# Kernel optimization log

Hardware: AMD Instinct MI355X
Metric: run time of the kernel (lower is better)

## Reference

```python
import jax, jax.numpy as jnp
import numpy as np

BATCH = 8192
GROUPS = 512
ARITY = 3
OUT_DIM = 8
ACT_FACTOR = 1.0


def setup_inputs() -> dict:
    key = jax.random.key(0)
    k1, k2 = jax.random.split(key)
    X = jax.random.normal(k1, (BATCH, GROUPS * ARITY), dtype=jnp.float32)
    params = jax.random.normal(k2, (GROUPS, 3 ** ARITY, OUT_DIM), dtype=jnp.float32)
    return {"X": X, "params": params}


def _high_order_act_b(A, params):
    # A: [B, G, r], params: [G, 3**r, D]
    r = A.shape[2]
    ref_ind = (3 ** r - 1) // 2  # sum_{i<r} 3**i
    A_abs = jnp.abs(A)
    A_ind = jnp.argsort(A_abs, axis=2)                      # [B,G,r] int
    A_sort = jnp.take_along_axis(A_abs, A_ind, axis=2)      # sorted |A|
    sgn = jnp.where(A >= 0, 1, -1).astype(jnp.int32)
    A_sgn = jnp.take_along_axis(sgn, A_ind, axis=2)         # signs in sorted order
    # simplex interpolation coefficients: smallest |A| then successive diffs
    coef = jnp.concatenate(
        [A_sort[:, :, :1], A_sort[:, :, 1:] - A_sort[:, :, :-1]], axis=2
    )  # [B,G,r]
    # base-3 index: suffix cumsum of sign * 3**orig_index, offset to center
    terms = A_sgn * (3 ** A_ind.astype(jnp.int32))
    params_A_ind = jnp.flip(jnp.cumsum(jnp.flip(terms, axis=2), axis=2), axis=2) + ref_ind  # [B,G,r]
    idx = jnp.transpose(params_A_ind, (1, 0, 2))            # [G,B,r]
    # gather params[g, idx[g,b,k], :] -> [G,B,r,D]
    gathered = jnp.take_along_axis(params[:, None, :, :], idx[..., None], axis=2)
    # einsum 'jikl,ijk->ijl' (torch) == 'gbrd,bgr->bgd'
    return jnp.einsum('gbrd,bgr->bgd', gathered, coef)


def reference(X, params):
    B = X.shape[0]
    A = X.reshape(B, GROUPS, ARITY)
    out1 = _high_order_act_b(A, params)                     # [B,G,D]
    return out1.reshape(B, GROUPS * OUT_DIM) * ACT_FACTOR
```

## Files before the change

### kernel.cpp

```cpp
#include <hip/hip_runtime.h>

typedef float vf4 __attribute__((ext_vector_type(4)));

#define BATCH  8192
#define GROUPS 512
#define OUT_D  8
#define GCH    32
#define NCH    (GROUPS / GCH)
#define RT     64
#define PQ     54
#define LQ     55

__global__ __launch_bounds__(256) void hoact_kernel(
    const float* __restrict__ X,
    const float* __restrict__ P,
    float* __restrict__ out)
{
    __shared__ vf4 lp[GCH * LQ];

    const int chunk = blockIdx.x % NCH;
    const int rt    = blockIdx.x / NCH;

    const int tid  = threadIdx.x;
    const int lane = tid & 63;
    const int w    = tid >> 6;
    const int gsub = lane >> 1;
    const int h    = lane & 1;

    const vf4* P4 = (const vf4*)P + (size_t)chunk * (GCH * PQ);
    #pragma unroll
    for (int k = 0; k < 7; ++k) {
        int m = tid + 256 * k;
        if (m < GCH * PQ) {
            int gq = m / PQ;
            int iq = m - gq * PQ;
            lp[gq * LQ + iq] = P4[m];
        }
    }
    __syncthreads();

    const int g = chunk * GCH + gsub;
    const float* xcol = X + (size_t)g * 3;
    vf4* outb = (vf4*)out + (size_t)chunk * (GCH * OUT_D / 4) + lane;
    const size_t row_u = GROUPS * OUT_D / 4;
    const int base = gsub * LQ + h;

    #pragma unroll
    for (int it = 0; it < RT / 4; ++it) {
        const int row = rt * RT + w * (RT / 4) + it;

        const float* xp = xcol + (size_t)row * (GROUPS * 3);
        float x0 = xp[0], x1 = xp[1], x2 = xp[2];

        float b0 = fabsf(x0), b1 = fabsf(x1), b2 = fabsf(x2);
        int t0 = (x0 >= 0.f) ? 1 : -1;
        int t1 = (x1 >= 0.f) ? 3 : -3;
        int t2 = (x2 >= 0.f) ? 9 : -9;
        if (b0 > b1) { float tb=b0; b0=b1; b1=tb; int tt=t0; t0=t1; t1=tt; }
        if (b1 > b2) { float tb=b1; b1=b2; b2=tb; int tt=t1; t1=t2; t2=tt; }
        if (b0 > b1) { float tb=b0; b0=b1; b1=tb; int tt=t0; t0=t1; t1=tt; }
        int i2 = t2 + 13;
        int i1 = t1 + t2 + 13;
        int i0 = t0 + t1 + t2 + 13;
        float c0 = b0;
        float c1 = b1 - b0;
        float c2 = b2 - b1;

        vf4 q0 = lp[base + i0 * 2];
        vf4 q1 = lp[base + i1 * 2];
        vf4 q2 = lp[base + i2 * 2];

        vf4 r = c0 * q0 + c1 * q1 + c2 * q2;

        __builtin_nontemporal_store(r, outb + (size_t)row * row_u);
    }
}

extern "C" void kernel_launch(void* const* d_in, const int* in_sizes, int n_in,
                              void* d_out, int out_size, void* d_ws, size_t ws_size,
                              hipStream_t stream) {
    const float* X = (const float*)d_in[0];
    const float* P = (const float*)d_in[1];
    float* out = (float*)d_out;

    const int grid = (BATCH / RT) * NCH;
    hoact_kernel<<<grid, 256, 0, stream>>>(X, P, out);
}
```

Measured before the change: 34.58 us.

## Use persistent grid-stride blocks with register prefetch of next X rows

```diff
diff --git a/kernel.cpp b/kernel.cpp
--- a/kernel.cpp
+++ b/kernel.cpp
@@ -7,7 +7,9 @@
 #define OUT_D  8
 #define GCH    32
 #define NCH    (GROUPS / GCH)
-#define RT     64
+#define NSLOT  80
+#define SR     8
+#define NSTR   (BATCH / SR)
 #define PQ     54
 #define LQ     55
 
@@ -19,7 +21,7 @@
     __shared__ vf4 lp[GCH * LQ];
 
     const int chunk = blockIdx.x % NCH;
-    const int rt    = blockIdx.x / NCH;
+    const int slot  = blockIdx.x / NCH;
 
     const int tid  = threadIdx.x;
     const int lane = tid & 63;
@@ -37,42 +39,67 @@
             lp[gq * LQ + iq] = P4[m];
         }
     }
+
+    const int g = chunk * GCH + gsub;
+    const float* xg = X + (size_t)g * 3;
+    const size_t xrow  = GROUPS * 3;
+    const size_t row_u = GROUPS * OUT_D / 4;
+    vf4* outg = (vf4*)out + (size_t)chunk * (GCH * OUT_D / 4) + lane;
+    const int base = gsub * LQ + h;
+
+    float xc[6];
+    {
+        int r0 = slot * SR + w * 2;
+        const float* xp0 = xg + (size_t)r0 * xrow;
+        const float* xp1 = xg + (size_t)(r0 + 1) * xrow;
+        xc[0] = xp0[0]; xc[1] = xp0[1]; xc[2] = xp0[2];
+        xc[3] = xp1[0]; xc[4] = xp1[1]; xc[5] = xp1[2];
+    }
+
     __syncthreads();
 
-    const int g = chunk * GCH + gsub;
-    const float* xcol = X + (size_t)g * 3;
-    vf4* outb = (vf4*)out + (size_t)chunk * (GCH * OUT_D / 4) + lane;
-    const size_t row_u = GROUPS * OUT_D / 4;
-    const int base = gsub * LQ + h;
+    #pragma unroll 1
+    for (int t = slot; t < NSTR; t += NSLOT) {
+        float xn[6];
+        const int tn = t + NSLOT;
+        if (tn < NSTR) {
+            int r0 = tn * SR + w * 2;
+            const float* xp0 = xg + (size_t)r0 * xrow;
+            const float* xp1 = xg + (size_t)(r0 + 1) * xrow;
+            xn[0] = xp0[0]; xn[1] = xp0[1]; xn[2] = xp0[2];
+            xn[3] = xp1[0]; xn[4] = xp1[1]; xn[5] = xp1[2];
+        }
 
-    #pragma unroll
-    for (int it = 0; it < RT / 4; ++it) {
-        const int row = rt * RT + w * (RT / 4) + it;
+        #pragma unroll
+        for (int rr = 0; rr < 2; ++rr) {
+            float x0 = xc[rr*3+0], x1 = xc[rr*3+1], x2 = xc[rr*3+2];
 
-        const float* xp = xcol + (size_t)row * (GROUPS * 3);
-        float x0 = xp[0], x1 = xp[1], x2 = xp[2];
+            float b0 = fabsf(x0), b1 = fabsf(x1), b2 = fabsf(x2);
+            int t0 = (x0 >= 0.f) ? 1 : -1;
+            int t1 = (x1 >= 0.f) ? 3 : -3;
+            int t2 = (x2 >= 0.f) ? 9 : -9;
+            if (b0 > b1) { float tb=b0; b0=b1; b1=tb; int tt=t0; t0=t1; t1=tt; }
+            if (b1 > b2) { float tb=b1; b1=b2; b2=tb; int tt=t1; t1=t2; t2=tt; }
+            if (b0 > b1) { float tb=b0; b0=b1; b1=tb; int tt=t0; t0=t1; t1=tt; }
+            int i2 = t2 + 13;
+            int i1 = t1 + t2 + 13;
+            int i0 = t0 + t1 + t2 + 13;
+            float c0 = b0;
+            float c1 = b1 - b0;
+            float c2 = b2 - b1;
 
-        float b0 = fabsf(x0), b1 = fabsf(x1), b2 = fabsf(x2);
-        int t0 = (x0 >= 0.f) ? 1 : -1;
-        int t1 = (x1 >= 0.f) ? 3 : -3;
-        int t2 = (x2 >= 0.f) ? 9 : -9;
-        if (b0 > b1) { float tb=b0; b0=b1; b1=tb; int tt=t0; t0=t1; t1=tt; }
-        if (b1 > b2) { float tb=b1; b1=b2; b2=tb; int tt=t1; t1=t2; t2=tt; }
-        if (b0 > b1) { float tb=b0; b0=b1; b1=tb; int tt=t0; t0=t1; t1=tt; }
-        int i2 = t2 + 13;
-        int i1 = t1 + t2 + 13;
-        int i0 = t0 + t1 + t2 + 13;
-        float c0 = b0;
-        float c1 = b1 - b0;
-        float c2 = b2 - b1;
+            vf4 q0 = lp[base + i0 * 2];
+            vf4 q1 = lp[base + i1 * 2];
+            vf4 q2 = lp[base + i2 * 2];
 
-        vf4 q0 = lp[base + i0 * 2];
-        vf4 q1 = lp[base + i1 * 2];
-        vf4 q2 = lp[base + i2 * 2];
+            vf4 r = c0 * q0 + c1 * q1 + c2 * q2;
 
-        vf4 r = c0 * q0 + c1 * q1 + c2 * q2;
+            int row = t * SR + w * 2 + rr;
+            __builtin_nontemporal_store(r, outg + (size_t)row * row_u);
+        }
 
-        __builtin_nontemporal_store(r, outb + (size_t)row * row_u);
+        #pragma unroll
+        for (int q = 0; q < 6; ++q) xc[q] = xn[q];
     }
 }
 
@@ -83,6 +110,6 @@
     const float* P = (const float*)d_in[1];
     float* out = (float*)d_out;
 
-    const int grid = (BATCH / RT) * NCH;
+    const int grid = NCH * NSLOT;
     hoact_kernel<<<grid, 256, 0, stream>>>(X, P, out);
 }
```

Result: no change. 34.45 us (-0.4%).
